# Kernel tuning notes

Measured on AMD Instinct MI355X. Metric: run time of the kernel, lower is better.

Reference implementation:

```python
import jax, jax.numpy as jnp
import numpy as np

DIM = 256
HID = 128


def setup_inputs() -> dict:
    key = jax.random.key(0)
    ks = jax.random.split(key, 10)
    B, T = 8, 2048
    s_in = 1.0 / np.sqrt(DIM)
    s_h = 1.0 / np.sqrt(HID)
    return {
        "x": jax.random.normal(ks[0], (B, T, DIM), jnp.float32),
        "adapt_bias": jax.random.normal(ks[1], (B, T, T), jnp.float32),
        "Wq": jax.random.uniform(ks[2], (HID, DIM), jnp.float32, -s_in, s_in),
        "bq": jax.random.uniform(ks[3], (HID,), jnp.float32, -s_in, s_in),
        "Wk": jax.random.uniform(ks[4], (HID, DIM), jnp.float32, -s_in, s_in),
        "bk": jax.random.uniform(ks[5], (HID,), jnp.float32, -s_in, s_in),
        "Wv": jax.random.uniform(ks[6], (HID, DIM), jnp.float32, -s_in, s_in),
        "bv": jax.random.uniform(ks[7], (HID,), jnp.float32, -s_in, s_in),
        "Wp": jax.random.uniform(ks[8], (DIM, HID), jnp.float32, -s_h, s_h),
        "bp": jax.random.uniform(ks[9], (DIM,), jnp.float32, -s_h, s_h),
    }


def reference(x, adapt_bias, Wq, bq, Wk, bk, Wv, bv, Wp, bp):
    # y = x (default). Q,K,V: [B,T,H]
    Q = jnp.einsum('btd,hd->bth', x, Wq) + bq
    K = jnp.einsum('btd,hd->bth', x, Wk) + bk
    V = jnp.einsum('btd,hd->bth', x, Wv) + bv
    Q_sig = jax.nn.sigmoid(Q)
    ab = jax.nn.softmax(adapt_bias, axis=-1)        # [B,T,T]
    Ksm = jax.nn.softmax(K, axis=1)                 # softmax over time dim
    eab = jnp.exp(ab)                               # [B,T,T]
    eK = jnp.exp(Ksm)                               # [B,T,H]
    num = jnp.einsum('bts,bsh->bth', eab, eK * V)
    den = jnp.einsum('bts,bsh->bth', eab, eK)
    Yt = Q_sig * (num / den)                        # [B,T,H]
    return jnp.einsum('bth,dh->btd', Yt, Wp) + bp   # [B,T,DIM]
```

## Files before the change

kernel.cpp:

```cpp
#include <hip/hip_runtime.h>
#include <hip/hip_bf16.h>

#define B_ 8
#define T_ 2048
#define D_ 256
#define H_ 128

typedef float f32x4 __attribute__((ext_vector_type(4)));
typedef short bf16x8 __attribute__((ext_vector_type(8)));

__device__ __forceinline__ unsigned short f2bf(float f){
  union { float f; unsigned u; } v; v.f = f;
  unsigned u = v.u;
  unsigned r = (u + 0x7FFFu + ((u >> 16) & 1u)) >> 16;
  return (unsigned short)r;
}

#define GLL16(g, l) __builtin_amdgcn_global_load_lds( \
    (const __attribute__((address_space(1))) void*)(g), \
    (__attribute__((address_space(3))) void*)(l), 16, 0, 0)

__device__ __forceinline__ float blk_reduce(float v, bool is_max, float* sbuf){
  for(int o = 32; o > 0; o >>= 1){
    float t = __shfl_xor(v, o);
    v = is_max ? fmaxf(v, t) : (v + t);
  }
  int w = threadIdx.x >> 6;
  __syncthreads();
  if((threadIdx.x & 63) == 0) sbuf[w] = v;
  __syncthreads();
  float r = sbuf[0];
  for(int i = 1; i < 4; i++) r = is_max ? fmaxf(r, sbuf[i]) : (r + sbuf[i]);
  return r;
}

__global__ __launch_bounds__(256) void qkv_kernel(
    const float* __restrict__ x,
    const float* __restrict__ Wq, const float* __restrict__ bq,
    const float* __restrict__ Wk, const float* __restrict__ bk,
    const float* __restrict__ Wv, const float* __restrict__ bv,
    float* __restrict__ Qsig, float* __restrict__ Kt, float* __restrict__ Vt)
{
  const int mat = blockIdx.y;
  const int g0  = blockIdx.x * 64;
  const int tid = threadIdx.x;
  const float* W   = (mat == 0) ? Wq : (mat == 1) ? Wk : Wv;
  const float* bia = (mat == 0) ? bq : (mat == 1) ? bk : bv;

  __shared__ __align__(16) short As[64 * 32];
  __shared__ __align__(16) short Ws[128 * 32];
  __shared__ float tbuf[64][129];

  const int w = tid >> 6, lane = tid & 63, rl = lane & 15, kg = lane >> 4;
  f32x4 acc[8];
  for(int i = 0; i < 8; i++) acc[i] = (f32x4){0.f, 0.f, 0.f, 0.f};

  const int c = tid & 31, r8 = tid >> 5;
  for(int kk = 0; kk < 256; kk += 32){
    __syncthreads();
    for(int p = 0; p < 8; p++){
      int rr = r8 + p * 8;
      As[rr * 32 + c] = (short)f2bf(x[(size_t)(g0 + rr) * 256 + kk + c]);
    }
    for(int p = 0; p < 16; p++){
      int hh = r8 + p * 8;
      Ws[hh * 32 + c] = (short)f2bf(W[(size_t)hh * 256 + kk + c]);
    }
    __syncthreads();
    bf16x8 a = *(const bf16x8*)&As[(w * 16 + rl) * 32 + kg * 8];
    for(int cf = 0; cf < 8; cf++){
      bf16x8 bb = *(const bf16x8*)&Ws[(cf * 16 + rl) * 32 + kg * 8];
      acc[cf] = __builtin_amdgcn_mfma_f32_16x16x32_bf16(a, bb, acc[cf], 0, 0, 0);
    }
  }

  const int b = g0 >> 11, t0 = g0 & 2047;
  if(mat == 0){
    for(int cf = 0; cf < 8; cf++){
      int h = cf * 16 + rl;
      float bh = bia[h];
      for(int r = 0; r < 4; r++){
        int tl = w * 16 + kg * 4 + r;
        float v = acc[cf][r] + bh;
        Qsig[(size_t)(g0 + tl) * 128 + h] = 1.f / (1.f + __expf(-v));
      }
    }
  } else {
    for(int cf = 0; cf < 8; cf++){
      int h = cf * 16 + rl;
      float bh = bia[h];
      for(int r = 0; r < 4; r++){
        int tl = w * 16 + kg * 4 + r;
        tbuf[tl][h] = acc[cf][r] + bh;
      }
    }
    __syncthreads();
    float* dst = (mat == 1) ? Kt : Vt;
    int h = tid >> 1, part = tid & 1;
    float* drow = dst + (size_t)(b * 128 + h) * 2048 + t0 + part * 32;
    for(int i = 0; i < 32; i += 4){
      float4 o;
      o.x = tbuf[part * 32 + i + 0][h];
      o.y = tbuf[part * 32 + i + 1][h];
      o.z = tbuf[part * 32 + i + 2][h];
      o.w = tbuf[part * 32 + i + 3][h];
      *(float4*)(drow + i) = o;
    }
  }
}

__global__ __launch_bounds__(256) void colsm_kernel(
    const float* __restrict__ Kt, const float* __restrict__ Vt,
    unsigned short* __restrict__ Mt)
{
  __shared__ float sbuf[4];
  const int b  = blockIdx.x >> 5;
  const int hg = blockIdx.x & 31;
  const int tid = threadIdx.x;
  for(int i = 0; i < 4; i++){
    int h = hg * 4 + i;
    const float* kr = Kt + (size_t)(b * 128 + h) * 2048;
    const float* vr = Vt + (size_t)(b * 128 + h) * 2048;
    float4 k0 = *(const float4*)(kr + tid * 4);
    float4 k1 = *(const float4*)(kr + tid * 4 + 1024);
    float m = fmaxf(fmaxf(fmaxf(k0.x, k0.y), fmaxf(k0.z, k0.w)),
                    fmaxf(fmaxf(k1.x, k1.y), fmaxf(k1.z, k1.w)));
    m = blk_reduce(m, true, sbuf);
    float s = __expf(k0.x - m) + __expf(k0.y - m) + __expf(k0.z - m) + __expf(k0.w - m)
            + __expf(k1.x - m) + __expf(k1.y - m) + __expf(k1.z - m) + __expf(k1.w - m);
    s = blk_reduce(s, false, sbuf);
    float iz = 1.f / s;
    float4 v0 = *(const float4*)(vr + tid * 4);
    float4 v1 = *(const float4*)(vr + tid * 4 + 1024);
    unsigned short* ekvp = Mt + (size_t)(b * 256 + h) * 2048;
    unsigned short* ekp  = Mt + (size_t)(b * 256 + 128 + h) * 2048;
    ushort4 pv, pe;
    float e;
    e = __expf(__expf(k0.x - m) * iz); pv.x = f2bf(e * v0.x); pe.x = f2bf(e);
    e = __expf(__expf(k0.y - m) * iz); pv.y = f2bf(e * v0.y); pe.y = f2bf(e);
    e = __expf(__expf(k0.z - m) * iz); pv.z = f2bf(e * v0.z); pe.z = f2bf(e);
    e = __expf(__expf(k0.w - m) * iz); pv.w = f2bf(e * v0.w); pe.w = f2bf(e);
    ((ushort4*)ekvp)[tid] = pv;
    ((ushort4*)ekp)[tid]  = pe;
    e = __expf(__expf(k1.x - m) * iz); pv.x = f2bf(e * v1.x); pe.x = f2bf(e);
    e = __expf(__expf(k1.y - m) * iz); pv.y = f2bf(e * v1.y); pe.y = f2bf(e);
    e = __expf(__expf(k1.z - m) * iz); pv.z = f2bf(e * v1.z); pe.z = f2bf(e);
    e = __expf(__expf(k1.w - m) * iz); pv.w = f2bf(e * v1.w); pe.w = f2bf(e);
    ((ushort4*)ekvp)[tid + 256] = pv;
    ((ushort4*)ekp)[tid + 256]  = pe;
  }
}

__global__ __launch_bounds__(256) void softexp_kernel(
    const float* __restrict__ ab, unsigned short* __restrict__ eab)
{
  __shared__ float sbuf[4];
  const size_t row = blockIdx.x;
  const float* r = ab + row * 2048;
  const int tid = threadIdx.x;
  float4 v0 = *(const float4*)(r + tid * 4);
  float4 v1 = *(const float4*)(r + tid * 4 + 1024);
  float m = fmaxf(fmaxf(fmaxf(v0.x, v0.y), fmaxf(v0.z, v0.w)),
                  fmaxf(fmaxf(v1.x, v1.y), fmaxf(v1.z, v1.w)));
  m = blk_reduce(m, true, sbuf);
  float e0x = __expf(v0.x - m), e0y = __expf(v0.y - m);
  float e0z = __expf(v0.z - m), e0w = __expf(v0.w - m);
  float e1x = __expf(v1.x - m), e1y = __expf(v1.y - m);
  float e1z = __expf(v1.z - m), e1w = __expf(v1.w - m);
  float s = e0x + e0y + e0z + e0w + e1x + e1y + e1z + e1w;
  s = blk_reduce(s, false, sbuf);
  float iz = 1.f / s;
  ushort4 o;
  o.x = f2bf(__expf(e0x * iz)); o.y = f2bf(__expf(e0y * iz));
  o.z = f2bf(__expf(e0z * iz)); o.w = f2bf(__expf(e0w * iz));
  *(ushort4*)(eab + row * 2048 + tid * 4) = o;
  o.x = f2bf(__expf(e1x * iz)); o.y = f2bf(__expf(e1y * iz));
  o.z = f2bf(__expf(e1z * iz)); o.w = f2bf(__expf(e1w * iz));
  *(ushort4*)(eab + row * 2048 + tid * 4 + 1024) = o;
}

__global__ __launch_bounds__(256) void aft_gemm2(
    const unsigned short* __restrict__ eab,
    const unsigned short* __restrict__ Mt,
    const float* __restrict__ Qsig,
    unsigned short* __restrict__ Yt)
{
  __shared__ __align__(16) unsigned short As2[2][32 * 64];
  __shared__ __align__(16) unsigned short Bs2[2][256 * 64];

  const int bid = blockIdx.x;
  const int swz = (bid & 7) * 64 + (bid >> 3);
  const int b   = swz >> 6;
  const int t0  = (swz & 63) * 32;

  const int tid = threadIdx.x;
  const int w = tid >> 6, lane = tid & 63;
  const int rl = lane & 15, kg = lane >> 4;

  const int lr = lane >> 3;
  const int cc = (lane & 7) ^ lr;

  const size_t rowbase = (size_t)b * 2048 + t0;
  const unsigned short* a_src = eab + (rowbase + (size_t)(w * 8 + lr)) * 2048 + cc * 8;
  const unsigned short* b_src = Mt + ((size_t)b * 256 + w * 64 + lr) * 2048 + cc * 8;

  f32x4 acc[2][4];
#pragma unroll
  for(int i = 0; i < 2; i++)
#pragma unroll
    for(int j = 0; j < 4; j++) acc[i][j] = (f32x4){0.f, 0.f, 0.f, 0.f};

  auto stage = [&](int buf, int t){
    GLL16(a_src + t * 64, &As2[buf][w * 512]);
#pragma unroll
    for(int i = 0; i < 8; i++)
      GLL16(b_src + i * 16384 + t * 64, &Bs2[buf][w * 4096 + i * 512]);
  };

  const int rx = rl & 7;
  stage(0, 0);
  __syncthreads();

  for(int t = 0; t < 32; ++t){
    const int cur = t & 1;
    if(t < 31) stage(cur ^ 1, t + 1);
#pragma unroll
    for(int ks = 0; ks < 2; ++ks){
      const int slot = ((ks * 4 + kg) ^ rx) * 8;
      bf16x8 a0 = *(const bf16x8*)&As2[cur][rl * 64 + slot];
      bf16x8 a1 = *(const bf16x8*)&As2[cur][(16 + rl) * 64 + slot];
#pragma unroll
      for(int cf = 0; cf < 4; ++cf){
        const int crow = ((cf < 2) ? (w * 32 + cf * 16)
                                   : (128 + w * 32 + (cf - 2) * 16)) + rl;
        bf16x8 bb = *(const bf16x8*)&Bs2[cur][crow * 64 + slot];
        acc[0][cf] = __builtin_amdgcn_mfma_f32_16x16x32_bf16(a0, bb, acc[0][cf], 0, 0, 0);
        acc[1][cf] = __builtin_amdgcn_mfma_f32_16x16x32_bf16(a1, bb, acc[1][cf], 0, 0, 0);
      }
    }
    __syncthreads();
  }

#pragma unroll
  for(int rf = 0; rf < 2; ++rf)
#pragma unroll
    for(int cf = 0; cf < 2; ++cf){
      const int h = w * 32 + cf * 16 + rl;
#pragma unroll
      for(int r = 0; r < 4; ++r){
        const int tl = rf * 16 + kg * 4 + r;
        const size_t g = rowbase + tl;
        float num = acc[rf][cf][r], den = acc[rf][cf + 2][r];
        float q = Qsig[g * 128 + h];
        Yt[g * 128 + h] = f2bf(q * num / den);
      }
    }
}

__global__ __launch_bounds__(256) void outproj_kernel(
    const unsigned short* __restrict__ Yt, const float* __restrict__ Wp,
    const float* __restrict__ bp, float* __restrict__ out)
{
  __shared__ __align__(16) short As[64 * 32];
  __shared__ __align__(16) short Bs[256 * 32];
  const int g0 = blockIdx.x * 64;
  const int tid = threadIdx.x;
  const int w = tid >> 6, lane = tid & 63, rl = lane & 15, kg = lane >> 4;
  f32x4 acc[16];
  for(int i = 0; i < 16; i++) acc[i] = (f32x4){0.f, 0.f, 0.f, 0.f};

  const int ar = tid >> 2, apart = tid & 3;
  const int c = tid & 31, dr = tid >> 5;
  for(int k = 0; k < 128; k += 32){
    __syncthreads();
    *(uint4*)&As[ar * 32 + apart * 8] =
        *(const uint4*)(Yt + (size_t)(g0 + ar) * 128 + k + apart * 8);
    for(int p = 0; p < 32; p++){
      int d = dr + p * 8;
      Bs[d * 32 + c] = (short)f2bf(Wp[(size_t)d * 128 + k + c]);
    }
    __syncthreads();
    bf16x8 a = *(const bf16x8*)&As[(w * 16 + rl) * 32 + kg * 8];
    for(int cf = 0; cf < 16; cf++){
      bf16x8 bb = *(const bf16x8*)&Bs[(cf * 16 + rl) * 32 + kg * 8];
      acc[cf] = __builtin_amdgcn_mfma_f32_16x16x32_bf16(a, bb, acc[cf], 0, 0, 0);
    }
  }
  for(int cf = 0; cf < 16; cf++){
    int d = cf * 16 + rl;
    float bpd = bp[d];
    for(int r = 0; r < 4; r++){
      int tl = w * 16 + kg * 4 + r;
      out[(size_t)(g0 + tl) * 256 + d] = acc[cf][r] + bpd;
    }
  }
}

extern "C" void kernel_launch(void* const* d_in, const int* in_sizes, int n_in,
                              void* d_out, int out_size, void* d_ws, size_t ws_size,
                              hipStream_t stream)
{
  const float* x  = (const float*)d_in[0];
  const float* ab = (const float*)d_in[1];
  const float* Wq = (const float*)d_in[2];
  const float* bq = (const float*)d_in[3];
  const float* Wk = (const float*)d_in[4];
  const float* bk = (const float*)d_in[5];
  const float* Wv = (const float*)d_in[6];
  const float* bv = (const float*)d_in[7];
  const float* Wp = (const float*)d_in[8];
  const float* bp = (const float*)d_in[9];
  float* out = (float*)d_out;

  char* ws = (char*)d_ws;
  float* Qsig          = (float*)(ws);
  float* Kt            = (float*)(ws + 8388608);
  float* Vt            = (float*)(ws + 16777216);
  unsigned short* Mt   = (unsigned short*)(ws + 25165824);
  unsigned short* eab  = (unsigned short*)(ws + 33554432);
  unsigned short* Yt   = (unsigned short*)(ws + 8388608);

  qkv_kernel<<<dim3(256, 3), 256, 0, stream>>>(x, Wq, bq, Wk, bk, Wv, bv, Qsig, Kt, Vt);
  colsm_kernel<<<256, 256, 0, stream>>>(Kt, Vt, Mt);
  softexp_kernel<<<16384, 256, 0, stream>>>(ab, eab);
  aft_gemm2<<<512, 256, 0, stream>>>(eab, Mt, Qsig, Yt);
  outproj_kernel<<<256, 256, 0, stream>>>(Yt, Wp, bp, out);
}
```

Before: 105.6 us.

## Retile aft GEMM to 64-row by 64-head tiles with 2x2 wave grid

Changes the per-block tile of the eab x Mt GEMM from 32 rows by all 128 heads (256 Mt rows) to 64 rows by half the heads (128 Mt rows), with waves arranged 2x2. Each block now loads half as many bytes per K step (A 8KB + B 16KB instead of A 4KB + B 32KB), cutting Mt re-reads while eab rows are read twice across head halves. LDS per block also drops, which may allow more resident blocks. The block-to-batch mapping also changes, interleaving batches across consecutive block ids.

```diff
diff --git a/kernel.cpp b/kernel.cpp
--- a/kernel.cpp
+++ b/kernel.cpp
@@ -179,30 +179,35 @@
   *(ushort4*)(eab + row * 2048 + tid * 4 + 1024) = o;
 }
 
-__global__ __launch_bounds__(256) void aft_gemm2(
+__global__ __launch_bounds__(256) void aft_gemm3(
     const unsigned short* __restrict__ eab,
     const unsigned short* __restrict__ Mt,
     const float* __restrict__ Qsig,
     unsigned short* __restrict__ Yt)
 {
-  __shared__ __align__(16) unsigned short As2[2][32 * 64];
-  __shared__ __align__(16) unsigned short Bs2[2][256 * 64];
+  __shared__ __align__(16) unsigned short As2[2][64 * 64];
+  __shared__ __align__(16) unsigned short Bs2[2][128 * 64];
 
   const int bid = blockIdx.x;
-  const int swz = (bid & 7) * 64 + (bid >> 3);
-  const int b   = swz >> 6;
-  const int t0  = (swz & 63) * 32;
+  const int b   = bid & 7;
+  const int idx = bid >> 3;
+  const int rt  = idx >> 1;
+  const int hb  = idx & 1;
+  const int t0  = rt * 64;
+  const int h0  = hb * 64;
 
   const int tid = threadIdx.x;
   const int w = tid >> 6, lane = tid & 63;
   const int rl = lane & 15, kg = lane >> 4;
+  const int wr = w >> 1, wc = w & 1;
 
   const int lr = lane >> 3;
   const int cc = (lane & 7) ^ lr;
 
   const size_t rowbase = (size_t)b * 2048 + t0;
-  const unsigned short* a_src = eab + (rowbase + (size_t)(w * 8 + lr)) * 2048 + cc * 8;
-  const unsigned short* b_src = Mt + ((size_t)b * 256 + w * 64 + lr) * 2048 + cc * 8;
+  const unsigned short* a_src = eab + (rowbase + (size_t)(w * 16 + lr)) * 2048 + cc * 8;
+  const int mtrow = (w < 2) ? (h0 + w * 32 + lr) : (128 + h0 + (w - 2) * 32 + lr);
+  const unsigned short* b_src = Mt + ((size_t)b * 256 + mtrow) * 2048 + cc * 8;
 
   f32x4 acc[2][4];
 #pragma unroll
@@ -211,10 +216,12 @@
     for(int j = 0; j < 4; j++) acc[i][j] = (f32x4){0.f, 0.f, 0.f, 0.f};
 
   auto stage = [&](int buf, int t){
-    GLL16(a_src + t * 64, &As2[buf][w * 512]);
-#pragma unroll
-    for(int i = 0; i < 8; i++)
-      GLL16(b_src + i * 16384 + t * 64, &Bs2[buf][w * 4096 + i * 512]);
+#pragma unroll
+    for(int i = 0; i < 2; i++)
+      GLL16(a_src + (size_t)i * 8 * 2048 + t * 64, &As2[buf][(w * 16 + i * 8) * 64]);
+#pragma unroll
+    for(int i = 0; i < 4; i++)
+      GLL16(b_src + (size_t)i * 8 * 2048 + t * 64, &Bs2[buf][(w * 32 + i * 8) * 64]);
   };
 
   const int rx = rl & 7;
@@ -227,13 +234,13 @@
 #pragma unroll
     for(int ks = 0; ks < 2; ++ks){
       const int slot = ((ks * 4 + kg) ^ rx) * 8;
-      bf16x8 a0 = *(const bf16x8*)&As2[cur][rl * 64 + slot];
-      bf16x8 a1 = *(const bf16x8*)&As2[cur][(16 + rl) * 64 + slot];
+      bf16x8 a0 = *(const bf16x8*)&As2[cur][(wr * 32 + rl) * 64 + slot];
+      bf16x8 a1 = *(const bf16x8*)&As2[cur][(wr * 32 + 16 + rl) * 64 + slot];
 #pragma unroll
       for(int cf = 0; cf < 4; ++cf){
-        const int crow = ((cf < 2) ? (w * 32 + cf * 16)
-                                   : (128 + w * 32 + (cf - 2) * 16)) + rl;
-        bf16x8 bb = *(const bf16x8*)&Bs2[cur][crow * 64 + slot];
+        const int brow = ((cf < 2) ? (wc * 32 + cf * 16)
+                                   : (64 + wc * 32 + (cf - 2) * 16)) + rl;
+        bf16x8 bb = *(const bf16x8*)&Bs2[cur][brow * 64 + slot];
         acc[0][cf] = __builtin_amdgcn_mfma_f32_16x16x32_bf16(a0, bb, acc[0][cf], 0, 0, 0);
         acc[1][cf] = __builtin_amdgcn_mfma_f32_16x16x32_bf16(a1, bb, acc[1][cf], 0, 0, 0);
       }
@@ -245,10 +252,10 @@
   for(int rf = 0; rf < 2; ++rf)
 #pragma unroll
     for(int cf = 0; cf < 2; ++cf){
-      const int h = w * 32 + cf * 16 + rl;
+      const int h = h0 + wc * 32 + cf * 16 + rl;
 #pragma unroll
       for(int r = 0; r < 4; ++r){
-        const int tl = rf * 16 + kg * 4 + r;
+        const int tl = wr * 32 + rf * 16 + kg * 4 + r;
         const size_t g = rowbase + tl;
         float num = acc[rf][cf][r], den = acc[rf][cf + 2][r];
         float q = Qsig[g * 128 + h];
@@ -323,6 +330,6 @@
   qkv_kernel<<<dim3(256, 3), 256, 0, stream>>>(x, Wq, bq, Wk, bk, Wv, bv, Qsig, Kt, Vt);
   colsm_kernel<<<256, 256, 0, stream>>>(Kt, Vt, Mt);
   softexp_kernel<<<16384, 256, 0, stream>>>(ab, eab);
-  aft_gemm2<<<512, 256, 0, stream>>>(eab, Mt, Qsig, Yt);
+  aft_gemm3<<<512, 256, 0, stream>>>(eab, Mt, Qsig, Yt);
   outproj_kernel<<<256, 256, 0, stream>>>(Yt, Wp, bp, out);
 }
```

Result: faster. 103.2 us (-2.2%).
